# Kernel optimization log

Measured on AMD Instinct MI355X. Metric: run time of the kernel, lower is better.

## Reference

```python
import jax, jax.numpy as jnp
import numpy as np

N = 200000
E = 500000
F_IN = 165
HID = 256
N_CLASSES = 2


def setup_inputs() -> dict:
    key = jax.random.key(0)
    ks = jax.random.split(key, 8)
    x = jax.random.normal(ks[0], (N, F_IN), dtype=jnp.float32)
    edge_index = jax.random.randint(ks[1], (2, E), 0, N, dtype=jnp.int64)
    # PyG SAGEConv params: lin_l applied to mean-aggregated neighbors (with bias),
    # lin_r applied to root features (no bias). Glorot-ish init scale.
    def lin(k, fin, fout):
        return jax.random.normal(k, (fin, fout), dtype=jnp.float32) / np.sqrt(fin)
    return {
        "x": x,
        "edge_index": edge_index,
        "w1_l": lin(ks[2], F_IN, HID),
        "w1_r": lin(ks[3], F_IN, HID),
        "b1": jnp.zeros((HID,), dtype=jnp.float32),
        "w2_l": lin(ks[4], HID, N_CLASSES),
        "w2_r": lin(ks[5], HID, N_CLASSES),
        "b2": jnp.zeros((N_CLASSES,), dtype=jnp.float32),
    }


def _sage_conv(x, edge_index, w_l, w_r, b):
    # PyG SAGEConv with default mean aggregation:
    #   out = lin_l(mean_{j in N(i)} x_j) + lin_r(x_i) + b
    src, dst = edge_index[0], edge_index[1]
    n = x.shape[0]
    deg = jax.ops.segment_sum(jnp.ones((src.shape[0],), x.dtype), dst, num_segments=n)
    agg = jax.ops.segment_sum(x[src], dst, num_segments=n)  # [N, F]
    agg = agg / jnp.maximum(deg, 1.0)[:, None]
    return agg @ w_l + x @ w_r + b


def reference(x, edge_index, w1_l, w1_r, b1, w2_l, w2_r, b2):
    h = jax.nn.relu(_sage_conv(x, edge_index, w1_l, w1_r, b1))
    # F.dropout(training=self.training) is identity in eval mode.
    logits = _sage_conv(h, edge_index, w2_l, w2_r, b2)
    return (logits, edge_index)
```

## Files before the change

### kernel.cpp

```cpp
#include <hip/hip_runtime.h>
#include <hip/hip_bf16.h>
#include <hip/hip_fp16.h>

#define N_NODES 200000
#define N_EDGES 500000
#define F_IN    165
#define HID     256
#define SX      192
#define NB      782

typedef float    floatx4 __attribute__((ext_vector_type(4)));
typedef float    floatx4a __attribute__((ext_vector_type(4), aligned(16)));
typedef float    float4u __attribute__((ext_vector_type(4), aligned(4)));
typedef _Float16 half8   __attribute__((ext_vector_type(8)));

__global__ void cast_x_kernel(const float* __restrict__ x, half8* __restrict__ xh8) {
    int idx = blockIdx.x * blockDim.x + threadIdx.x;
    int row = idx / 24;
    int p = idx - row * 24;
    int f0 = p * 8;
    const float* px = x + (long)row * F_IN + f0;
    half8 r;
    if (f0 + 8 <= F_IN) {
        float4u lo = *(const float4u*)px;
        float4u hi = *(const float4u*)(px + 4);
#pragma unroll
        for (int q = 0; q < 4; ++q) r[q] = (_Float16)lo[q];
#pragma unroll
        for (int q = 0; q < 4; ++q) r[4 + q] = (_Float16)hi[q];
    } else {
#pragma unroll
        for (int q = 0; q < 8; ++q)
            r[q] = (f0 + q < F_IN) ? (_Float16)px[q] : (_Float16)0.0f;
    }
    xh8[idx] = r;
}

__global__ void hist_kernel(const int* __restrict__ ei, int* __restrict__ degi) {
    int e = blockIdx.x * blockDim.x + threadIdx.x;
    if (e < N_EDGES) atomicAdd(&degi[ei[N_EDGES + e]], 1);
}

__global__ __launch_bounds__(256) void block_sum_kernel(const int* __restrict__ degi,
                                                        int* __restrict__ bsum) {
    __shared__ int sh[256];
    int t = threadIdx.x, i = blockIdx.x * 256 + t;
    sh[t] = (i < N_NODES) ? degi[i] : 0;
    __syncthreads();
#pragma unroll
    for (int off = 128; off > 0; off >>= 1) {
        if (t < off) sh[t] += sh[t + off];
        __syncthreads();
    }
    if (t == 0) bsum[blockIdx.x] = sh[0];
}

__global__ __launch_bounds__(1024) void scan_bsum_kernel(const int* __restrict__ bsum,
                                                         int* __restrict__ boff,
                                                         int* __restrict__ row_start) {
    __shared__ int sh[1024];
    int t = threadIdx.x;
    int v = (t < NB) ? bsum[t] : 0;
    sh[t] = v;
    __syncthreads();
    for (int off = 1; off < 1024; off <<= 1) {
        int u = (t >= off) ? sh[t - off] : 0;
        __syncthreads();
        sh[t] += u;
        __syncthreads();
    }
    if (t < NB) boff[t] = sh[t] - v;
    if (t == 1023) row_start[N_NODES] = sh[1023];
}

__global__ __launch_bounds__(256) void scan_emit_kernel(const int* __restrict__ degi,
                                                        const int* __restrict__ boff,
                                                        int* __restrict__ row_start,
                                                        int* __restrict__ cursor,
                                                        float* __restrict__ invdeg) {
    __shared__ int sh[256];
    int t = threadIdx.x, i = blockIdx.x * 256 + t;
    int d = (i < N_NODES) ? degi[i] : 0;
    sh[t] = d;
    __syncthreads();
#pragma unroll
    for (int off = 1; off < 256; off <<= 1) {
        int u = (t >= off) ? sh[t - off] : 0;
        __syncthreads();
        sh[t] += u;
        __syncthreads();
    }
    if (i < N_NODES) {
        int row = boff[blockIdx.x] + sh[t] - d;
        row_start[i] = row;
        cursor[i] = row;
        invdeg[i] = 1.0f / fmaxf((float)d, 1.0f);
    }
}

__global__ void scatter_edges_kernel(const int* __restrict__ ei,
                                     int* __restrict__ cursor,
                                     int* __restrict__ csr) {
    int e = blockIdx.x * blockDim.x + threadIdx.x;
    if (e >= N_EDGES) return;
    int s = ei[e];
    int d = ei[N_EDGES + e];
    int pos = atomicAdd(&cursor[d], 1);
    csr[pos] = s;
}

__global__ void gather_agg_kernel(const half8* __restrict__ xh8,
                                  const int* __restrict__ row_start,
                                  const int* __restrict__ csr,
                                  half8* __restrict__ aggh8) {
    int idx = blockIdx.x * blockDim.x + threadIdx.x;
    int n = idx / 24;
    int p = idx - n * 24;
    int e0 = row_start[n], e1 = row_start[n + 1];
    half8 acc = {0, 0, 0, 0, 0, 0, 0, 0};
    half8 acc2 = {0, 0, 0, 0, 0, 0, 0, 0};
    int e = e0;
    for (; e + 2 <= e1; e += 2) {
        int s0 = csr[e], s1 = csr[e + 1];
        half8 v0 = xh8[(long)s0 * 24 + p];
        half8 v1 = xh8[(long)s1 * 24 + p];
        acc += v0;
        acc2 += v1;
    }
    if (e < e1) acc += xh8[(long)csr[e] * 24 + p];
    aggh8[idx] = acc + acc2;
}

__global__ void prep_bfrag_kernel(const float* __restrict__ w1l,
                                  const float* __restrict__ w1r,
                                  _Float16* __restrict__ bfrag) {
    int gid = blockIdx.x * blockDim.x + threadIdx.x;
    if (gid >= 12 * 16 * 64) return;
    int lane = gid & 63;
    int j = (gid >> 6) & 15;
    int c = gid >> 10;
    int quad = lane >> 4, n = lane & 15;
    const float* w = (c < 6) ? w1l : w1r;
    int kb = (c < 6 ? c : c - 6) * 32;
    int col = j * 16 + n;
    half8 r;
#pragma unroll
    for (int q = 0; q < 8; ++q) {
        int k = kb + quad * 8 + q;
        r[q] = (_Float16)((k < F_IN) ? w[k * HID + col] : 0.0f);
    }
    *(half8*)(bfrag + gid * 8) = r;
}

__global__ __launch_bounds__(512, 6) void gemm_fused_kernel(
        const _Float16* __restrict__ xh, const _Float16* __restrict__ aggh,
        const float* __restrict__ invdeg, const _Float16* __restrict__ bfrag,
        const float* __restrict__ b1,
        const float* __restrict__ w2l, const float* __restrict__ w2r,
        float* __restrict__ tl, float* __restrict__ tr) {
    __shared__ __attribute__((aligned(16))) _Float16 As[2][4096];
    __shared__ float tlr[64][4];
    const int tid = threadIdx.x;
    const int w = tid >> 6, lane = tid & 63;
    const int quad = lane >> 4, l15 = lane & 15;
    const int rowbase = blockIdx.x * 64;

    if (tid < 256) ((float*)tlr)[tid] = 0.0f;

    const int s = tid & 255;
    const int su = tid >> 8;
    const int srow_l = s >> 2;
    const int sseg = (s & 3) ^ ((srow_l >> 1) & 3);
    const int sgoff = (rowbase + srow_l) * SX + sseg * 8;
    const int ldst = su * 4096 + (w & 3) * 1024;

    int aoff[4];
#pragma unroll
    for (int nt = 0; nt < 4; ++nt) {
        int r = nt * 16 + l15;
        int slot = r * 4 + (quad ^ ((r >> 1) & 3));
        aoff[nt] = slot * 16;
    }
    const int boff = (2 * w * 64 + lane) * 16;

    float iv[4];
#pragma unroll
    for (int nt = 0; nt < 4; ++nt)
        iv[nt] = invdeg[rowbase + nt * 16 + l15];

    floatx4 acc[2][4];
#pragma unroll
    for (int i = 0; i < 2; ++i)
#pragma unroll
        for (int nt = 0; nt < 4; ++nt)
            acc[i][nt] = (floatx4){0.f, 0.f, 0.f, 0.f};

    auto STAGE = [&](int p) {
        const int cc = 2 * p + su;
        const _Float16* src = (cc < 6) ? aggh : xh;
        const int kb = (cc < 6 ? cc : cc - 6) * 32;
        const _Float16* gp = src + sgoff + kb;
        char* dst = (char*)(&As[p & 1][0]) + ldst;
        __builtin_amdgcn_global_load_lds(
            (const __attribute__((address_space(1))) void*)gp,
            (__attribute__((address_space(3))) void*)dst, 16, 0, 0);
    };

    STAGE(0);
    asm volatile("s_waitcnt vmcnt(0)" ::: "memory");
    __builtin_amdgcn_s_barrier();
    __builtin_amdgcn_sched_barrier(0);

#pragma unroll 1
    for (int t = 0; t < 6; ++t) {
        if (t < 5) STAGE(t + 1);
        const char* abase = (const char*)(&As[t & 1][0]);
#pragma unroll
        for (int u = 0; u < 2; ++u) {
            const int cc = 2 * t + u;
            half8 a[4], b[2];
#pragma unroll
            for (int nt = 0; nt < 4; ++nt)
                a[nt] = *(const half8*)(abase + u * 4096 + aoff[nt]);
#pragma unroll
            for (int i = 0; i < 2; ++i)
                b[i] = *(const half8*)((const char*)bfrag + boff + (cc * 16 + i) * 1024);
#pragma unroll
            for (int i = 0; i < 2; ++i)
#pragma unroll
                for (int nt = 0; nt < 4; ++nt)
                    acc[i][nt] = __builtin_amdgcn_mfma_f32_16x16x32_f16(b[i], a[nt], acc[i][nt], 0, 0, 0);
        }
        if (t == 2) {
#pragma unroll
            for (int nt = 0; nt < 4; ++nt)
#pragma unroll
                for (int i = 0; i < 2; ++i)
                    acc[i][nt] *= iv[nt];
        }
        asm volatile("s_waitcnt vmcnt(0)" ::: "memory");
        __builtin_amdgcn_s_barrier();
        __builtin_amdgcn_sched_barrier(0);
    }

    float sacc[4][4];
#pragma unroll
    for (int nt = 0; nt < 4; ++nt)
#pragma unroll
        for (int c = 0; c < 4; ++c) sacc[nt][c] = 0.0f;

#pragma unroll
    for (int i = 0; i < 2; ++i) {
        const int j0 = w * 32 + i * 16 + quad * 4;
        floatx4a bbv = *(const floatx4a*)(b1 + j0);
        floatx4a wlA = *(const floatx4a*)(w2l + j0 * 2);
        floatx4a wlB = *(const floatx4a*)(w2l + j0 * 2 + 4);
        floatx4a wrA = *(const floatx4a*)(w2r + j0 * 2);
        floatx4a wrB = *(const floatx4a*)(w2r + j0 * 2 + 4);
#pragma unroll
        for (int nt = 0; nt < 4; ++nt) {
#pragma unroll
            for (int reg = 0; reg < 4; ++reg) {
                float v = fmaxf(acc[i][nt][reg] + bbv[reg], 0.0f);
                float wl0 = (reg < 2) ? wlA[(reg & 1) * 2]     : wlB[(reg & 1) * 2];
                float wl1 = (reg < 2) ? wlA[(reg & 1) * 2 + 1] : wlB[(reg & 1) * 2 + 1];
                float wr0 = (reg < 2) ? wrA[(reg & 1) * 2]     : wrB[(reg & 1) * 2];
                float wr1 = (reg < 2) ? wrA[(reg & 1) * 2 + 1] : wrB[(reg & 1) * 2 + 1];
                sacc[nt][0] += v * wl0;
                sacc[nt][1] += v * wl1;
                sacc[nt][2] += v * wr0;
                sacc[nt][3] += v * wr1;
            }
        }
    }
#pragma unroll
    for (int nt = 0; nt < 4; ++nt) {
#pragma unroll
        for (int c = 0; c < 4; ++c) {
            sacc[nt][c] += __shfl_xor(sacc[nt][c], 16, 64);
            sacc[nt][c] += __shfl_xor(sacc[nt][c], 32, 64);
        }
        if (quad == 0) {
            int rl = nt * 16 + l15;
            atomicAdd(&tlr[rl][0], sacc[nt][0]);
            atomicAdd(&tlr[rl][1], sacc[nt][1]);
            atomicAdd(&tlr[rl][2], sacc[nt][2]);
            atomicAdd(&tlr[rl][3], sacc[nt][3]);
        }
    }
    __syncthreads();
    if (tid < 64) {
        int row = rowbase + tid;
        tl[row * 2 + 0] = tlr[tid][0];
        tl[row * 2 + 1] = tlr[tid][1];
        tr[row * 2 + 0] = tlr[tid][2];
        tr[row * 2 + 1] = tlr[tid][3];
    }
}

__global__ void gather_out_kernel(const int* __restrict__ row_start,
                                  const int* __restrict__ csr,
                                  const float* __restrict__ tl,
                                  const float* __restrict__ tr,
                                  const float* __restrict__ invdeg,
                                  const float* __restrict__ b2,
                                  float* __restrict__ out) {
    int i = blockIdx.x * blockDim.x + threadIdx.x;
    if (i >= N_NODES) return;
    int e0 = row_start[i], e1 = row_start[i + 1];
    float a0 = 0.f, a1 = 0.f;
    for (int e = e0; e < e1; ++e) {
        int s = csr[e];
        a0 += tl[s * 2 + 0];
        a1 += tl[s * 2 + 1];
    }
    float inv = invdeg[i];
    out[i * 2 + 0] = a0 * inv + tr[i * 2 + 0] + b2[0];
    out[i * 2 + 1] = a1 * inv + tr[i * 2 + 1] + b2[1];
}

__global__ void cast_edges_kernel(const int* __restrict__ ei,
                                  float* __restrict__ out) {
    int i = blockIdx.x * blockDim.x + threadIdx.x;
    if (i < 2 * N_EDGES) out[i] = (float)ei[i];
}

extern "C" void kernel_launch(void* const* d_in, const int* in_sizes, int n_in,
                              void* d_out, int out_size, void* d_ws, size_t ws_size,
                              hipStream_t stream) {
    const float* x    = (const float*)d_in[0];
    const int*   ei   = (const int*)d_in[1];
    const float* w1_l = (const float*)d_in[2];
    const float* w1_r = (const float*)d_in[3];
    const float* b1   = (const float*)d_in[4];
    const float* w2_l = (const float*)d_in[5];
    const float* w2_r = (const float*)d_in[6];
    const float* b2   = (const float*)d_in[7];

    char* ws = (char*)d_ws;
    int*   degi      = (int*)(ws);
    int*   row_start = (int*)(ws + 800000);
    int*   cursor    = (int*)(ws + 1600032);
    float* invdeg    = (float*)(ws + 2400032);
    int*   csr       = (int*)(ws + 3200032);
    float* tl        = (float*)(ws + 5200032);
    float* tr        = (float*)(ws + 6800032);
    int*   bsum      = (int*)(ws + 8400032);
    int*   boff      = (int*)(ws + 8403232);
    _Float16* bfrag  = (_Float16*)(ws + 8406432);
    _Float16* aggh   = (_Float16*)(ws + 8610000);
    _Float16* xh     = (_Float16*)(ws + 85410000);

    float* out = (float*)d_out;

    (void)hipMemsetAsync(degi, 0, 800000, stream);

    cast_x_kernel<<<(N_NODES * 24) / 256, 256, 0, stream>>>(x, (half8*)xh);
    prep_bfrag_kernel<<<48, 256, 0, stream>>>(w1_l, w1_r, bfrag);

    hist_kernel<<<(N_EDGES + 255) / 256, 256, 0, stream>>>(ei, degi);
    block_sum_kernel<<<NB, 256, 0, stream>>>(degi, bsum);
    scan_bsum_kernel<<<1, 1024, 0, stream>>>(bsum, boff, row_start);
    scan_emit_kernel<<<NB, 256, 0, stream>>>(degi, boff, row_start, cursor, invdeg);
    scatter_edges_kernel<<<(N_EDGES + 255) / 256, 256, 0, stream>>>(ei, cursor, csr);

    gather_agg_kernel<<<(N_NODES * 24) / 256, 256, 0, stream>>>(
        (const half8*)xh, row_start, csr, (half8*)aggh);

    gemm_fused_kernel<<<N_NODES / 64, 512, 0, stream>>>(
        xh, aggh, invdeg, bfrag, b1, w2_l, w2_r, tl, tr);

    gather_out_kernel<<<NB, 256, 0, stream>>>(row_start, csr, tl, tr, invdeg, b2, out);
    cast_edges_kernel<<<(2 * N_EDGES + 255) / 256, 256, 0, stream>>>(ei, out + 2 * N_NODES);
}
```

Measured before the change: 431.1 us.

## Stage A tiles via registers instead of direct-to-LDS loads, cache epilogue weights in LDS

Measured after the change: 444.1 us. 1.03x slower.

```diff
diff --git a/kernel.cpp b/kernel.cpp
--- a/kernel.cpp
+++ b/kernel.cpp
@@ -159,6 +159,7 @@
         const float* __restrict__ w2l, const float* __restrict__ w2r,
         float* __restrict__ tl, float* __restrict__ tr) {
     __shared__ __attribute__((aligned(16))) _Float16 As[2][4096];
+    __shared__ float wtab[1280];
     __shared__ float tlr[64][4];
     const int tid = threadIdx.x;
     const int w = tid >> 6, lane = tid & 63;
@@ -166,13 +167,16 @@
     const int rowbase = blockIdx.x * 64;
 
     if (tid < 256) ((float*)tlr)[tid] = 0.0f;
+#pragma unroll
+    for (int q = tid; q < 1280; q += 512)
+        wtab[q] = (q < 256) ? b1[q] : ((q < 768) ? w2l[q - 256] : w2r[q - 768]);
 
     const int s = tid & 255;
     const int su = tid >> 8;
     const int srow_l = s >> 2;
     const int sseg = (s & 3) ^ ((srow_l >> 1) & 3);
     const int sgoff = (rowbase + srow_l) * SX + sseg * 8;
-    const int ldst = su * 4096 + (w & 3) * 1024;
+    const int sdst = su * 4096 + s * 16;
 
     int aoff[4];
 #pragma unroll
@@ -195,25 +199,23 @@
         for (int nt = 0; nt < 4; ++nt)
             acc[i][nt] = (floatx4){0.f, 0.f, 0.f, 0.f};
 
-    auto STAGE = [&](int p) {
+    auto LOADG = [&](int p) -> half8 {
         const int cc = 2 * p + su;
         const _Float16* src = (cc < 6) ? aggh : xh;
         const int kb = (cc < 6 ? cc : cc - 6) * 32;
-        const _Float16* gp = src + sgoff + kb;
-        char* dst = (char*)(&As[p & 1][0]) + ldst;
-        __builtin_amdgcn_global_load_lds(
-            (const __attribute__((address_space(1))) void*)gp,
-            (__attribute__((address_space(3))) void*)dst, 16, 0, 0);
+        return *(const half8*)(src + sgoff + kb);
     };
 
-    STAGE(0);
-    asm volatile("s_waitcnt vmcnt(0)" ::: "memory");
-    __builtin_amdgcn_s_barrier();
-    __builtin_amdgcn_sched_barrier(0);
+    half8 r = LOADG(0);
 
 #pragma unroll 1
     for (int t = 0; t < 6; ++t) {
-        if (t < 5) STAGE(t + 1);
+        *(half8*)((char*)(&As[t & 1][0]) + sdst) = r;
+        if (t < 5) r = LOADG(t + 1);
+        asm volatile("s_waitcnt lgkmcnt(0)" ::: "memory");
+        __builtin_amdgcn_s_barrier();
+        __builtin_amdgcn_sched_barrier(0);
+
         const char* abase = (const char*)(&As[t & 1][0]);
 #pragma unroll
         for (int u = 0; u < 2; ++u) {
@@ -238,54 +240,38 @@
                 for (int i = 0; i < 2; ++i)
                     acc[i][nt] *= iv[nt];
         }
-        asm volatile("s_waitcnt vmcnt(0)" ::: "memory");
-        __builtin_amdgcn_s_barrier();
-        __builtin_amdgcn_sched_barrier(0);
-    }
-
-    float sacc[4][4];
-#pragma unroll
-    for (int nt = 0; nt < 4; ++nt)
-#pragma unroll
-        for (int c = 0; c < 4; ++c) sacc[nt][c] = 0.0f;
-
-#pragma unroll
-    for (int i = 0; i < 2; ++i) {
-        const int j0 = w * 32 + i * 16 + quad * 4;
-        floatx4a bbv = *(const floatx4a*)(b1 + j0);
-        floatx4a wlA = *(const floatx4a*)(w2l + j0 * 2);
-        floatx4a wlB = *(const floatx4a*)(w2l + j0 * 2 + 4);
-        floatx4a wrA = *(const floatx4a*)(w2r + j0 * 2);
-        floatx4a wrB = *(const floatx4a*)(w2r + j0 * 2 + 4);
-#pragma unroll
-        for (int nt = 0; nt < 4; ++nt) {
+    }
+    __syncthreads();
+
+    const float* bt  = wtab;
+    const float* wlt = wtab + 256;
+    const float* wrt = wtab + 768;
+#pragma unroll
+    for (int nt = 0; nt < 4; ++nt) {
+        float s0 = 0.f, s1 = 0.f, s2 = 0.f, s3 = 0.f;
+#pragma unroll
+        for (int i = 0; i < 2; ++i) {
+            const int j0 = w * 32 + i * 16 + quad * 4;
 #pragma unroll
             for (int reg = 0; reg < 4; ++reg) {
-                float v = fmaxf(acc[i][nt][reg] + bbv[reg], 0.0f);
-                float wl0 = (reg < 2) ? wlA[(reg & 1) * 2]     : wlB[(reg & 1) * 2];
-                float wl1 = (reg < 2) ? wlA[(reg & 1) * 2 + 1] : wlB[(reg & 1) * 2 + 1];
-                float wr0 = (reg < 2) ? wrA[(reg & 1) * 2]     : wrB[(reg & 1) * 2];
-                float wr1 = (reg < 2) ? wrA[(reg & 1) * 2 + 1] : wrB[(reg & 1) * 2 + 1];
-                sacc[nt][0] += v * wl0;
-                sacc[nt][1] += v * wl1;
-                sacc[nt][2] += v * wr0;
-                sacc[nt][3] += v * wr1;
+                const int j = j0 + reg;
+                float v = fmaxf(acc[i][nt][reg] + bt[j], 0.0f);
+                s0 += v * wlt[2 * j];
+                s1 += v * wlt[2 * j + 1];
+                s2 += v * wrt[2 * j];
+                s3 += v * wrt[2 * j + 1];
             }
         }
-    }
-#pragma unroll
-    for (int nt = 0; nt < 4; ++nt) {
-#pragma unroll
-        for (int c = 0; c < 4; ++c) {
-            sacc[nt][c] += __shfl_xor(sacc[nt][c], 16, 64);
-            sacc[nt][c] += __shfl_xor(sacc[nt][c], 32, 64);
-        }
+        s0 += __shfl_xor(s0, 16, 64); s0 += __shfl_xor(s0, 32, 64);
+        s1 += __shfl_xor(s1, 16, 64); s1 += __shfl_xor(s1, 32, 64);
+        s2 += __shfl_xor(s2, 16, 64); s2 += __shfl_xor(s2, 32, 64);
+        s3 += __shfl_xor(s3, 16, 64); s3 += __shfl_xor(s3, 32, 64);
         if (quad == 0) {
             int rl = nt * 16 + l15;
-            atomicAdd(&tlr[rl][0], sacc[nt][0]);
-            atomicAdd(&tlr[rl][1], sacc[nt][1]);
-            atomicAdd(&tlr[rl][2], sacc[nt][2]);
-            atomicAdd(&tlr[rl][3], sacc[nt][3]);
+            atomicAdd(&tlr[rl][0], s0);
+            atomicAdd(&tlr[rl][1], s1);
+            atomicAdd(&tlr[rl][2], s2);
+            atomicAdd(&tlr[rl][3], s3);
         }
     }
     __syncthreads();
```

## Fuse neighbor mean-gather into the layer-1 GEMM, dropping the agg buffer

Applied to the files above, without the earlier changes.

Measured after the change: 426.8 us. Within noise of the previous version (-1.0%).

```diff
diff --git a/kernel.cpp b/kernel.cpp
--- a/kernel.cpp
+++ b/kernel.cpp
@@ -107,28 +107,6 @@
     int d = ei[N_EDGES + e];
     int pos = atomicAdd(&cursor[d], 1);
     csr[pos] = s;
-}
-
-__global__ void gather_agg_kernel(const half8* __restrict__ xh8,
-                                  const int* __restrict__ row_start,
-                                  const int* __restrict__ csr,
-                                  half8* __restrict__ aggh8) {
-    int idx = blockIdx.x * blockDim.x + threadIdx.x;
-    int n = idx / 24;
-    int p = idx - n * 24;
-    int e0 = row_start[n], e1 = row_start[n + 1];
-    half8 acc = {0, 0, 0, 0, 0, 0, 0, 0};
-    half8 acc2 = {0, 0, 0, 0, 0, 0, 0, 0};
-    int e = e0;
-    for (; e + 2 <= e1; e += 2) {
-        int s0 = csr[e], s1 = csr[e + 1];
-        half8 v0 = xh8[(long)s0 * 24 + p];
-        half8 v1 = xh8[(long)s1 * 24 + p];
-        acc += v0;
-        acc2 += v1;
-    }
-    if (e < e1) acc += xh8[(long)csr[e] * 24 + p];
-    aggh8[idx] = acc + acc2;
 }
 
 __global__ void prep_bfrag_kernel(const float* __restrict__ w1l,
@@ -152,8 +130,9 @@
     *(half8*)(bfrag + gid * 8) = r;
 }
 
-__global__ __launch_bounds__(512, 6) void gemm_fused_kernel(
-        const _Float16* __restrict__ xh, const _Float16* __restrict__ aggh,
+__global__ __launch_bounds__(512, 4) void gemm_fused_kernel(
+        const _Float16* __restrict__ xh,
+        const int* __restrict__ row_start, const int* __restrict__ csr,
         const float* __restrict__ invdeg, const _Float16* __restrict__ bfrag,
         const float* __restrict__ b1,
         const float* __restrict__ w2l, const float* __restrict__ w2r,
@@ -170,9 +149,11 @@
     const int s = tid & 255;
     const int su = tid >> 8;
     const int srow_l = s >> 2;
+    const int n = rowbase + srow_l;
     const int sseg = (s & 3) ^ ((srow_l >> 1) & 3);
-    const int sgoff = (rowbase + srow_l) * SX + sseg * 8;
-    const int ldst = su * 4096 + (w & 3) * 1024;
+    const int sgoff = n * SX + sseg * 8;
+    const int sdst = su * 4096 + s * 16;
+    const int e0 = row_start[n], e1 = row_start[n + 1];
 
     int aoff[4];
 #pragma unroll
@@ -195,25 +176,34 @@
         for (int nt = 0; nt < 4; ++nt)
             acc[i][nt] = (floatx4){0.f, 0.f, 0.f, 0.f};
 
-    auto STAGE = [&](int p) {
-        const int cc = 2 * p + su;
-        const _Float16* src = (cc < 6) ? aggh : xh;
-        const int kb = (cc < 6 ? cc : cc - 6) * 32;
-        const _Float16* gp = src + sgoff + kb;
-        char* dst = (char*)(&As[p & 1][0]) + ldst;
-        __builtin_amdgcn_global_load_lds(
-            (const __attribute__((address_space(1))) void*)gp,
-            (__attribute__((address_space(3))) void*)dst, 16, 0, 0);
+    auto GATHER = [&](int p) -> half8 {
+        const int off = (2 * p + su) * 32 + sseg * 8;
+        half8 a0 = {0, 0, 0, 0, 0, 0, 0, 0};
+        half8 a1 = {0, 0, 0, 0, 0, 0, 0, 0};
+        int e = e0;
+        for (; e + 2 <= e1; e += 2) {
+            int s0 = csr[e], s1 = csr[e + 1];
+            a0 += *(const half8*)(xh + s0 * SX + off);
+            a1 += *(const half8*)(xh + s1 * SX + off);
+        }
+        if (e < e1) a0 += *(const half8*)(xh + csr[e] * SX + off);
+        return a0 + a1;
     };
-
-    STAGE(0);
-    asm volatile("s_waitcnt vmcnt(0)" ::: "memory");
-    __builtin_amdgcn_s_barrier();
-    __builtin_amdgcn_sched_barrier(0);
+    auto LOADR = [&](int p) -> half8 {
+        const int kb = (2 * p + su - 6) * 32;
+        return *(const half8*)(xh + sgoff + kb);
+    };
+
+    half8 r = GATHER(0);
 
 #pragma unroll 1
     for (int t = 0; t < 6; ++t) {
-        if (t < 5) STAGE(t + 1);
+        *(half8*)((char*)(&As[t & 1][0]) + sdst) = r;
+        if (t < 5) r = (t < 2) ? GATHER(t + 1) : LOADR(t + 1);
+        asm volatile("s_waitcnt lgkmcnt(0)" ::: "memory");
+        __builtin_amdgcn_s_barrier();
+        __builtin_amdgcn_sched_barrier(0);
+
         const char* abase = (const char*)(&As[t & 1][0]);
 #pragma unroll
         for (int u = 0; u < 2; ++u) {
@@ -238,9 +228,6 @@
                 for (int i = 0; i < 2; ++i)
                     acc[i][nt] *= iv[nt];
         }
-        asm volatile("s_waitcnt vmcnt(0)" ::: "memory");
-        __builtin_amdgcn_s_barrier();
-        __builtin_amdgcn_sched_barrier(0);
     }
 
     float sacc[4][4];
@@ -348,7 +335,6 @@
     int*   bsum      = (int*)(ws + 8400032);
     int*   boff      = (int*)(ws + 8403232);
     _Float16* bfrag  = (_Float16*)(ws + 8406432);
-    _Float16* aggh   = (_Float16*)(ws + 8610000);
     _Float16* xh     = (_Float16*)(ws + 85410000);
 
     float* out = (float*)d_out;
@@ -364,11 +350,8 @@
     scan_emit_kernel<<<NB, 256, 0, stream>>>(degi, boff, row_start, cursor, invdeg);
     scatter_edges_kernel<<<(N_EDGES + 255) / 256, 256, 0, stream>>>(ei, cursor, csr);
 
-    gather_agg_kernel<<<(N_NODES * 24) / 256, 256, 0, stream>>>(
-        (const half8*)xh, row_start, csr, (half8*)aggh);
-
     gemm_fused_kernel<<<N_NODES / 64, 512, 0, stream>>>(
-        xh, aggh, invdeg, bfrag, b1, w2_l, w2_r, tl, tr);
+        xh, row_start, csr, invdeg, bfrag, b1, w2_l, w2_r, tl, tr);
 
     gather_out_kernel<<<NB, 256, 0, stream>>>(row_start, csr, tl, tr, invdeg, b2, out);
     cast_edges_kernel<<<(2 * N_EDGES + 255) / 256, 256, 0, stream>>>(ei, out + 2 * N_NODES);
```
